# Kernel optimization log

Measured on AMD Instinct MI355X. Metric: run time of the kernel, lower is better.

Reference implementation:

```python
import jax, jax.numpy as jnp
import numpy as np

NUM_HEADS = 14
NUM_KV_HEADS = 2
HEAD_DIM = 64
HIDDEN = 896
ROPE_THETA = 1000000.0
NEG_INF = -1e9


def _rope_tables(seq_len, dtype=jnp.float32):
    inv_freq = 1.0 / (ROPE_THETA ** (jnp.arange(0, HEAD_DIM, 2, dtype=jnp.float32) / HEAD_DIM))
    t = jnp.arange(seq_len, dtype=jnp.float32)
    freqs = t[:, None] * inv_freq[None, :]          # [S, hd/2]
    emb = jnp.concatenate((freqs, freqs), axis=-1)  # [S, hd]
    return jnp.cos(emb).astype(dtype), jnp.sin(emb).astype(dtype)


def _rotate_half(x):
    x1, x2 = x[..., : x.shape[-1] // 2], x[..., x.shape[-1] // 2 :]
    return jnp.concatenate((-x2, x1), axis=-1)


def setup_inputs() -> dict:
    key = jax.random.key(0)
    ks = jax.random.split(key, 6)
    B, S = 2, 2048
    hidden_states = jax.random.normal(ks[0], (B, S, HIDDEN), dtype=jnp.float32)
    # additive causal mask [1, 1, S, S]
    causal = jnp.tril(jnp.ones((S, S), dtype=bool))
    attention_mask = jnp.where(causal, 0.0, NEG_INF).astype(jnp.float32)[None, None]
    sd = 1.0 / np.sqrt(HIDDEN)
    Wq = jax.random.normal(ks[1], (HIDDEN, NUM_HEADS * HEAD_DIM), dtype=jnp.float32) * sd
    bq = jnp.zeros((NUM_HEADS * HEAD_DIM,), dtype=jnp.float32)
    Wk = jax.random.normal(ks[2], (HIDDEN, NUM_KV_HEADS * HEAD_DIM), dtype=jnp.float32) * sd
    bk = jnp.zeros((NUM_KV_HEADS * HEAD_DIM,), dtype=jnp.float32)
    Wv = jax.random.normal(ks[3], (HIDDEN, NUM_KV_HEADS * HEAD_DIM), dtype=jnp.float32) * sd
    bv = jnp.zeros((NUM_KV_HEADS * HEAD_DIM,), dtype=jnp.float32)
    Wo = jax.random.normal(ks[4], (NUM_HEADS * HEAD_DIM, HIDDEN), dtype=jnp.float32) * sd
    return {
        'hidden_states': hidden_states, 'attention_mask': attention_mask,
        'Wq': Wq, 'bq': bq, 'Wk': Wk, 'bk': bk, 'Wv': Wv, 'bv': bv, 'Wo': Wo,
    }


def reference(hidden_states, attention_mask, Wq, bq, Wk, bk, Wv, bv, Wo):
    B, S, _ = hidden_states.shape
    n_groups = NUM_HEADS // NUM_KV_HEADS
    q = (hidden_states @ Wq + bq).reshape(B, S, NUM_HEADS, HEAD_DIM)
    k = (hidden_states @ Wk + bk).reshape(B, S, NUM_KV_HEADS, HEAD_DIM)
    v = (hidden_states @ Wv + bv).reshape(B, S, NUM_KV_HEADS, HEAD_DIM)

    cos, sin = _rope_tables(S, hidden_states.dtype)
    cos = cos[None, :, None, :]
    sin = sin[None, :, None, :]
    q = q * cos + _rotate_half(q) * sin
    k = k * cos + _rotate_half(k) * sin

    # GQA: repeat kv heads to match query heads
    k = jnp.repeat(k, n_groups, axis=2)  # [B, S, nH, hd]
    v = jnp.repeat(v, n_groups, axis=2)

    q = q.transpose(0, 2, 1, 3)  # [B, nH, S, hd]
    k = k.transpose(0, 2, 1, 3)
    v = v.transpose(0, 2, 1, 3)

    scores = jnp.einsum('bhqd,bhkd->bhqk', q, k) / jnp.sqrt(jnp.float32(HEAD_DIM)).astype(q.dtype)
    scores = scores + attention_mask
    attn = jax.nn.softmax(scores, axis=-1)
    out = jnp.einsum('bhqk,bhkd->bhqd', attn, v)        # [B, nH, S, hd]
    out = out.transpose(0, 2, 1, 3).reshape(B, S, -1)   # [B, S, nH*hd]
    return out @ Wo
```

## Files before the change

kernel.cpp:

```cpp
#include <hip/hip_runtime.h>
#include <hip/hip_bf16.h>
#include <math.h>

#define NH 14
#define NKV 2
#define HD 64
#define HID 896
#define SEQ 2048
#define BATCH 2
#define KT 28

typedef __attribute__((ext_vector_type(8))) short short8;
typedef __attribute__((ext_vector_type(4))) float f32x4;
typedef unsigned short ushort_t;

__device__ __forceinline__ unsigned short f2b(float f) {
    unsigned int u = __float_as_uint(f);
    unsigned int r = (u + 0x7fffu + ((u >> 16) & 1u)) >> 16;
    return (unsigned short)r;
}

__global__ __launch_bounds__(256) void xcast_kernel(
    const float* __restrict__ X, ushort_t* __restrict__ Xb)
{
    size_t i = ((size_t)blockIdx.x * 256 + threadIdx.x) * 8;
    float4 a = *(const float4*)(X + i);
    float4 b = *(const float4*)(X + i + 4);
    short8 o;
    o[0] = f2b(a.x); o[1] = f2b(a.y); o[2] = f2b(a.z); o[3] = f2b(a.w);
    o[4] = f2b(b.x); o[5] = f2b(b.y); o[6] = f2b(b.z); o[7] = f2b(b.w);
    *(short8*)(Xb + i) = o;
}

__global__ __launch_bounds__(256) void wtrans_kernel(
    const float* __restrict__ Wq, const float* __restrict__ Wk,
    const float* __restrict__ Wv, const float* __restrict__ Wo,
    ushort_t* __restrict__ WqkvT, ushort_t* __restrict__ WoT)
{
    __shared__ float tile[32][33];
    const int tx = threadIdx.x, ty = threadIdx.y;
    const int z = blockIdx.z;
    const float* src; ushort_t* dst; int N, rowoff;
    if      (z == 0) { src = Wq; dst = WqkvT; N = HID; rowoff = 0;    }
    else if (z == 1) { src = Wk; dst = WqkvT; N = 128; rowoff = 896;  }
    else if (z == 2) { src = Wv; dst = WqkvT; N = 128; rowoff = 1024; }
    else             { src = Wo; dst = WoT;   N = HID; rowoff = 0;    }
    const int k0 = blockIdx.x * 32;
    const int n0 = blockIdx.y * 32;
    if (n0 >= N) return;
    #pragma unroll
    for (int i = 0; i < 4; ++i)
        tile[ty * 4 + i][tx] = src[(size_t)(k0 + ty * 4 + i) * N + n0 + tx];
    __syncthreads();
    #pragma unroll
    for (int i = 0; i < 4; ++i)
        dst[(size_t)(rowoff + n0 + ty * 4 + i) * HID + k0 + tx]
            = f2b(tile[tx][ty * 4 + i]);
}

#define LDA 40
__global__ __launch_bounds__(256) void qkv_kernel(
    const ushort_t* __restrict__ Xb, const ushort_t* __restrict__ WqkvT,
    const float* __restrict__ bq, const float* __restrict__ bk,
    const float* __restrict__ bv,
    ushort_t* __restrict__ qbuf, ushort_t* __restrict__ kbuf,
    ushort_t* __restrict__ vbuf)
{
    __shared__ ushort_t Asb[2][128 * LDA];
    __shared__ ushort_t Bsb[2][64 * LDA];
    const int tid  = threadIdx.x;
    const int w    = tid >> 6;
    const int lane = tid & 63;
    const int quad = lane >> 4;
    const int l16  = lane & 15;
    const int m0 = blockIdx.x * 128;
    const int nt = blockIdx.y;
    const int nb = nt * 64;

    const int ar0 = tid >> 2;
    const int ac8 = tid & 3;
    const ushort_t* Ag0 = Xb + (size_t)(m0 + ar0) * HID + ac8 * 8;
    const ushort_t* Ag1 = Xb + (size_t)(m0 + ar0 + 64) * HID + ac8 * 8;
    const ushort_t* Bg  = WqkvT + (size_t)(nb + ar0) * HID + ac8 * 8;

    f32x4 acc[2][4];
    #pragma unroll
    for (int mf = 0; mf < 2; ++mf)
        #pragma unroll
        for (int nf = 0; nf < 4; ++nf) acc[mf][nf] = (f32x4){0.f, 0.f, 0.f, 0.f};

    short8 aReg0, aReg1, bReg;
    aReg0 = *(const short8*)(Ag0);
    aReg1 = *(const short8*)(Ag1);
    bReg  = *(const short8*)(Bg);
    *(short8*)&Asb[0][ar0 * LDA + ac8 * 8]        = aReg0;
    *(short8*)&Asb[0][(ar0 + 64) * LDA + ac8 * 8] = aReg1;
    *(short8*)&Bsb[0][ar0 * LDA + ac8 * 8]        = bReg;
    aReg0 = *(const short8*)(Ag0 + 32);
    aReg1 = *(const short8*)(Ag1 + 32);
    bReg  = *(const short8*)(Bg  + 32);

    for (int ks = 0; ks < KT; ++ks) {
        __syncthreads();
        const int cur = ks & 1;
        if (ks + 1 < KT) {
            *(short8*)&Asb[cur ^ 1][ar0 * LDA + ac8 * 8]        = aReg0;
            *(short8*)&Asb[cur ^ 1][(ar0 + 64) * LDA + ac8 * 8] = aReg1;
            *(short8*)&Bsb[cur ^ 1][ar0 * LDA + ac8 * 8]        = bReg;
        }
        if (ks + 2 < KT) {
            aReg0 = *(const short8*)(Ag0 + (ks + 2) * 32);
            aReg1 = *(const short8*)(Ag1 + (ks + 2) * 32);
            bReg  = *(const short8*)(Bg  + (ks + 2) * 32);
        }
        const ushort_t* Ab = &Asb[cur][(w * 32 + l16) * LDA + quad * 8];
        short8 a0 = *(const short8*)Ab;
        short8 a1 = *(const short8*)(Ab + 16 * LDA);
        #pragma unroll
        for (int nf = 0; nf < 4; ++nf) {
            short8 bf = *(const short8*)&Bsb[cur][(nf * 16 + l16) * LDA + quad * 8];
            acc[0][nf] = __builtin_amdgcn_mfma_f32_16x16x32_bf16(a0, bf, acc[0][nf], 0, 0, 0);
            acc[1][nf] = __builtin_amdgcn_mfma_f32_16x16x32_bf16(a1, bf, acc[1][nf], 0, 0, 0);
        }
    }

    float bcol[4];
    #pragma unroll
    for (int f = 0; f < 4; ++f) {
        int d = f * 16 + l16;
        bcol[f] = (nt < 14) ? bq[nt * 64 + d]
                : (nt < 16) ? bk[(nt - 14) * 64 + d]
                            : bv[(nt - 16) * 64 + d];
    }
    const float lnth = 13.815510558f;
    float if0 = expf(-((float)l16)        / 32.0f * lnth);
    float if1 = expf(-((float)(l16 + 16)) / 32.0f * lnth);

    #pragma unroll
    for (int mf = 0; mf < 2; ++mf)
        #pragma unroll
        for (int r = 0; r < 4; ++r) {
            int grow = m0 + w * 32 + mf * 16 + quad * 4 + r;
            int b = grow >> 11;
            int s = grow & 2047;
            float v0 = acc[mf][0][r] + bcol[0];
            float v1 = acc[mf][1][r] + bcol[1];
            float v2 = acc[mf][2][r] + bcol[2];
            float v3 = acc[mf][3][r] + bcol[3];
            if (nt < 16) {
                float s0, c0, s1, c1;
                sincosf((float)s * if0, &s0, &c0);
                sincosf((float)s * if1, &s1, &c1);
                float n0 = v0 * c0 - v2 * s0;
                float n2 = v2 * c0 + v0 * s0;
                float n1 = v1 * c1 - v3 * s1;
                float n3 = v3 * c1 + v1 * s1;
                v0 = n0; v1 = n1; v2 = n2; v3 = n3;
            }
            if (nt < 14) {
                ushort_t* dst = qbuf + ((size_t)(b * NH + nt) * SEQ + s) * HD;
                dst[l16]      = f2b(v0);
                dst[l16 + 16] = f2b(v1);
                dst[l16 + 32] = f2b(v2);
                dst[l16 + 48] = f2b(v3);
            } else if (nt < 16) {
                ushort_t* dst = kbuf + ((size_t)(b * NKV + nt - 14) * SEQ + s) * HD;
                dst[l16]      = f2b(v0);
                dst[l16 + 16] = f2b(v1);
                dst[l16 + 32] = f2b(v2);
                dst[l16 + 48] = f2b(v3);
            } else {
                ushort_t* dst = vbuf + (size_t)(b * NKV + nt - 16) * HD * SEQ + s;
                dst[(size_t)(l16)      * SEQ] = f2b(v0);
                dst[(size_t)(l16 + 16) * SEQ] = f2b(v1);
                dst[(size_t)(l16 + 32) * SEQ] = f2b(v2);
                dst[(size_t)(l16 + 48) * SEQ] = f2b(v3);
            }
        }
}

#define LDP 76
__global__ __launch_bounds__(256) void attn_kernel(
    const ushort_t* __restrict__ qbuf, const ushort_t* __restrict__ kbuf,
    const ushort_t* __restrict__ vbuf, ushort_t* __restrict__ abuf)
{
    __shared__ ushort_t Ks[64 * LDP];
    __shared__ ushort_t Vt[64 * LDP];
    __shared__ ushort_t Ps[4][16 * LDP];

    const int tid  = threadIdx.x;
    const int w    = tid >> 6;
    const int lane = tid & 63;
    const int quad = lane >> 4;
    const int l16  = lane & 15;
    const int bi = blockIdx.x;
    const int h  = blockIdx.y;
    const int b  = blockIdx.z;
    const int kvh = h / (NH / NKV);

    const ushort_t* kb_h = kbuf + (size_t)(b * NKV + kvh) * SEQ * HD;
    const ushort_t* vt_h = vbuf + (size_t)(b * NKV + kvh) * HD * SEQ;

    for (int pass = 0; pass < 2; ++pass) {
        const int qt = pass ? (31 - bi) : bi;

        const ushort_t* qrow =
            qbuf + ((size_t)((b * NH + h) * SEQ) + qt * 64 + w * 16 + l16) * HD;
        short8 qf0 = *(const short8*)(qrow + quad * 8);
        short8 qf1 = *(const short8*)(qrow + 32 + quad * 8);

        f32x4 O[4];
        float m_i[4], l_i[4];
        #pragma unroll
        for (int n = 0; n < 4; ++n) O[n] = (f32x4){0.f, 0.f, 0.f, 0.f};
        #pragma unroll
        for (int r = 0; r < 4; ++r) { m_i[r] = -1e30f; l_i[r] = 0.0f; }

        for (int kt = 0; kt <= qt; ++kt) {
            __syncthreads();
            for (int i = tid; i < 512; i += 256) {
                int row = i >> 3, c8 = i & 7;
                *(short8*)&Ks[row * LDP + c8 * 8] =
                    *(const short8*)(kb_h + ((size_t)(kt * 64 + row)) * HD + c8 * 8);
                *(short8*)&Vt[row * LDP + c8 * 8] =
                    *(const short8*)(vt_h + (size_t)row * SEQ + kt * 64 + c8 * 8);
            }
            __syncthreads();

            f32x4 S[4];
            #pragma unroll
            for (int f = 0; f < 4; ++f) {
                S[f] = (f32x4){0.f, 0.f, 0.f, 0.f};
                short8 kf0 = *(const short8*)&Ks[(f * 16 + l16) * LDP + quad * 8];
                short8 kf1 = *(const short8*)&Ks[(f * 16 + l16) * LDP + 32 + quad * 8];
                S[f] = __builtin_amdgcn_mfma_f32_16x16x32_bf16(qf0, kf0, S[f], 0, 0, 0);
                S[f] = __builtin_amdgcn_mfma_f32_16x16x32_bf16(qf1, kf1, S[f], 0, 0, 0);
            }

            const bool diag = (kt == qt);
            float sc[4][4];
            #pragma unroll
            for (int f = 0; f < 4; ++f)
                #pragma unroll
                for (int r = 0; r < 4; ++r) {
                    float v = S[f][r] * 0.125f;
                    if (diag && (f * 16 + l16) > (w * 16 + quad * 4 + r)) v = -1e30f;
                    sc[f][r] = v;
                }

            float pm[4];
            #pragma unroll
            for (int r = 0; r < 4; ++r)
                pm[r] = fmaxf(fmaxf(sc[0][r], sc[1][r]), fmaxf(sc[2][r], sc[3][r]));
            #pragma unroll
            for (int off = 1; off < 16; off <<= 1)
                #pragma unroll
                for (int r = 0; r < 4; ++r)
                    pm[r] = fmaxf(pm[r], __shfl_xor(pm[r], off));

            float alpha[4], psum[4];
            #pragma unroll
            for (int r = 0; r < 4; ++r) {
                float mnew = fmaxf(m_i[r], pm[r]);
                alpha[r] = __expf(m_i[r] - mnew);
                m_i[r] = mnew;
                psum[r] = 0.0f;
            }
            #pragma unroll
            for (int f = 0; f < 4; ++f)
                #pragma unroll
                for (int r = 0; r < 4; ++r) {
                    float p = __expf(sc[f][r] - m_i[r]);
                    sc[f][r] = p;
                    psum[r] += p;
                }
            #pragma unroll
            for (int off = 1; off < 16; off <<= 1)
                #pragma unroll
                for (int r = 0; r < 4; ++r)
                    psum[r] += __shfl_xor(psum[r], off);
            #pragma unroll
            for (int r = 0; r < 4; ++r)
                l_i[r] = l_i[r] * alpha[r] + psum[r];
            #pragma unroll
            for (int n = 0; n < 4; ++n)
                #pragma unroll
                for (int r = 0; r < 4; ++r)
                    O[n][r] *= alpha[r];

            #pragma unroll
            for (int f = 0; f < 4; ++f)
                #pragma unroll
                for (int r = 0; r < 4; ++r)
                    Ps[w][(quad * 4 + r) * LDP + f * 16 + l16] = f2b(sc[f][r]);
            short8 pa0 = *(const short8*)&Ps[w][l16 * LDP + quad * 8];
            short8 pa1 = *(const short8*)&Ps[w][l16 * LDP + 32 + quad * 8];

            #pragma unroll
            for (int n = 0; n < 4; ++n) {
                short8 vf0 = *(const short8*)&Vt[(n * 16 + l16) * LDP + quad * 8];
                short8 vf1 = *(const short8*)&Vt[(n * 16 + l16) * LDP + 32 + quad * 8];
                O[n] = __builtin_amdgcn_mfma_f32_16x16x32_bf16(pa0, vf0, O[n], 0, 0, 0);
                O[n] = __builtin_amdgcn_mfma_f32_16x16x32_bf16(pa1, vf1, O[n], 0, 0, 0);
            }
        }

        float inv[4];
        #pragma unroll
        for (int r = 0; r < 4; ++r) inv[r] = 1.0f / l_i[r];
        #pragma unroll
        for (int n = 0; n < 4; ++n)
            #pragma unroll
            for (int r = 0; r < 4; ++r) {
                int rowg = qt * 64 + w * 16 + quad * 4 + r;
                abuf[(size_t)(b * SEQ + rowg) * HID + h * HD + n * 16 + l16]
                    = f2b(O[n][r] * inv[r]);
            }
    }
}

__global__ __launch_bounds__(256) void oproj_kernel(
    const ushort_t* __restrict__ A, const ushort_t* __restrict__ WoT,
    float* __restrict__ out)
{
    __shared__ ushort_t Asb[2][128 * LDA];
    __shared__ ushort_t Bsb[2][64 * LDA];
    const int tid  = threadIdx.x;
    const int w    = tid >> 6;
    const int lane = tid & 63;
    const int quad = lane >> 4;
    const int l16  = lane & 15;
    const int m0 = blockIdx.x * 128;
    const int n0 = blockIdx.y * 64;

    const int ar0 = tid >> 2;
    const int ac8 = tid & 3;
    const ushort_t* Ag0 = A + (size_t)(m0 + ar0) * HID + ac8 * 8;
    const ushort_t* Ag1 = A + (size_t)(m0 + ar0 + 64) * HID + ac8 * 8;
    const ushort_t* Bg  = WoT + (size_t)(n0 + ar0) * HID + ac8 * 8;

    f32x4 acc[2][4];
    #pragma unroll
    for (int mf = 0; mf < 2; ++mf)
        #pragma unroll
        for (int nf = 0; nf < 4; ++nf) acc[mf][nf] = (f32x4){0.f, 0.f, 0.f, 0.f};

    short8 aReg0, aReg1, bReg;
    aReg0 = *(const short8*)(Ag0);
    aReg1 = *(const short8*)(Ag1);
    bReg  = *(const short8*)(Bg);
    *(short8*)&Asb[0][ar0 * LDA + ac8 * 8]        = aReg0;
    *(short8*)&Asb[0][(ar0 + 64) * LDA + ac8 * 8] = aReg1;
    *(short8*)&Bsb[0][ar0 * LDA + ac8 * 8]        = bReg;
    aReg0 = *(const short8*)(Ag0 + 32);
    aReg1 = *(const short8*)(Ag1 + 32);
    bReg  = *(const short8*)(Bg  + 32);

    for (int ks = 0; ks < KT; ++ks) {
        __syncthreads();
        const int cur = ks & 1;
        if (ks + 1 < KT) {
            *(short8*)&Asb[cur ^ 1][ar0 * LDA + ac8 * 8]        = aReg0;
            *(short8*)&Asb[cur ^ 1][(ar0 + 64) * LDA + ac8 * 8] = aReg1;
            *(short8*)&Bsb[cur ^ 1][ar0 * LDA + ac8 * 8]        = bReg;
        }
        if (ks + 2 < KT) {
            aReg0 = *(const short8*)(Ag0 + (ks + 2) * 32);
            aReg1 = *(const short8*)(Ag1 + (ks + 2) * 32);
            bReg  = *(const short8*)(Bg  + (ks + 2) * 32);
        }
        const ushort_t* Ab = &Asb[cur][(w * 32 + l16) * LDA + quad * 8];
        short8 a0 = *(const short8*)Ab;
        short8 a1 = *(const short8*)(Ab + 16 * LDA);
        #pragma unroll
        for (int nf = 0; nf < 4; ++nf) {
            short8 bf = *(const short8*)&Bsb[cur][(nf * 16 + l16) * LDA + quad * 8];
            acc[0][nf] = __builtin_amdgcn_mfma_f32_16x16x32_bf16(a0, bf, acc[0][nf], 0, 0, 0);
            acc[1][nf] = __builtin_amdgcn_mfma_f32_16x16x32_bf16(a1, bf, acc[1][nf], 0, 0, 0);
        }
    }

    #pragma unroll
    for (int mf = 0; mf < 2; ++mf)
        #pragma unroll
        for (int r = 0; r < 4; ++r) {
            size_t rbase = (size_t)(m0 + w * 32 + mf * 16 + quad * 4 + r) * HID + n0;
            #pragma unroll
            for (int f = 0; f < 4; ++f)
                out[rbase + f * 16 + l16] = acc[mf][f][r];
        }
}

extern "C" void kernel_launch(void* const* d_in, const int* in_sizes, int n_in,
                              void* d_out, int out_size, void* d_ws, size_t ws_size,
                              hipStream_t stream) {
    const float* X  = (const float*)d_in[0];
    const float* Wq = (const float*)d_in[2];
    const float* bq = (const float*)d_in[3];
    const float* Wk = (const float*)d_in[4];
    const float* bk = (const float*)d_in[5];
    const float* Wv = (const float*)d_in[6];
    const float* bv = (const float*)d_in[7];
    const float* Wo = (const float*)d_in[8];
    float* out = (float*)d_out;

    ushort_t* ws    = (ushort_t*)d_ws;
    ushort_t* Xb    = ws;
    ushort_t* WqkvT = Xb    + 3670016;
    ushort_t* WoT   = WqkvT + 1032192;
    ushort_t* qbuf  = WoT   + 802816;
    ushort_t* kbuf  = qbuf  + 3670016;
    ushort_t* vbuf  = kbuf  + 524288;
    ushort_t* abufb = vbuf  + 524288;

    xcast_kernel<<<dim3(1792), 256, 0, stream>>>(X, Xb);
    wtrans_kernel<<<dim3(28, 28, 4), dim3(32, 8), 0, stream>>>(
        Wq, Wk, Wv, Wo, WqkvT, WoT);
    qkv_kernel<<<dim3(32, 18), 256, 0, stream>>>(
        Xb, WqkvT, bq, bk, bv, qbuf, kbuf, vbuf);
    attn_kernel<<<dim3(16, NH, BATCH), 256, 0, stream>>>(
        qbuf, kbuf, vbuf, abufb);
    oproj_kernel<<<dim3(32, 14), 256, 0, stream>>>(
        abufb, WoT, out);
}
```

Baseline: 209.5 us.

## Load K/V fragments directly from global, drop LDS staging and pass pairing

The attention kernel stops staging K and V tiles through shared memory with two block barriers per step. Each wave now loads its MFMA fragments straight from global memory, relying on cache reuse across waves. The grid doubles to one query tile per block instead of pairing tiles for load balance. The 1/sqrt(d) scale is folded into Q in the projection kernel, and softmax uses exp2 with a log2e prescale. Risks are redundant global/L2 traffic across the four waves and causal-imbalanced blocks.

```diff
diff --git a/kernel.cpp b/kernel.cpp
--- a/kernel.cpp
+++ b/kernel.cpp
@@ -18,6 +18,10 @@
     unsigned int u = __float_as_uint(f);
     unsigned int r = (u + 0x7fffu + ((u >> 16) & 1u)) >> 16;
     return (unsigned short)r;
+}
+
+__device__ __forceinline__ float exp2fast(float x) {
+    return __builtin_amdgcn_exp2f(x);
 }
 
 __global__ __launch_bounds__(256) void xcast_kernel(
@@ -158,6 +162,7 @@
                 v0 = n0; v1 = n1; v2 = n2; v3 = n3;
             }
             if (nt < 14) {
+                v0 *= 0.125f; v1 *= 0.125f; v2 *= 0.125f; v3 *= 0.125f;
                 ushort_t* dst = qbuf + ((size_t)(b * NH + nt) * SEQ + s) * HD;
                 dst[l16]      = f2b(v0);
                 dst[l16 + 16] = f2b(v1);
@@ -184,8 +189,6 @@
     const ushort_t* __restrict__ qbuf, const ushort_t* __restrict__ kbuf,
     const ushort_t* __restrict__ vbuf, ushort_t* __restrict__ abuf)
 {
-    __shared__ ushort_t Ks[64 * LDP];
-    __shared__ ushort_t Vt[64 * LDP];
     __shared__ ushort_t Ps[4][16 * LDP];
 
     const int tid  = threadIdx.x;
@@ -193,7 +196,7 @@
     const int lane = tid & 63;
     const int quad = lane >> 4;
     const int l16  = lane & 15;
-    const int bi = blockIdx.x;
+    const int qt = blockIdx.x;
     const int h  = blockIdx.y;
     const int b  = blockIdx.z;
     const int kvh = h / (NH / NKV);
@@ -201,122 +204,121 @@
     const ushort_t* kb_h = kbuf + (size_t)(b * NKV + kvh) * SEQ * HD;
     const ushort_t* vt_h = vbuf + (size_t)(b * NKV + kvh) * HD * SEQ;
 
-    for (int pass = 0; pass < 2; ++pass) {
-        const int qt = pass ? (31 - bi) : bi;
-
-        const ushort_t* qrow =
-            qbuf + ((size_t)((b * NH + h) * SEQ) + qt * 64 + w * 16 + l16) * HD;
-        short8 qf0 = *(const short8*)(qrow + quad * 8);
-        short8 qf1 = *(const short8*)(qrow + 32 + quad * 8);
-
-        f32x4 O[4];
-        float m_i[4], l_i[4];
-        #pragma unroll
-        for (int n = 0; n < 4; ++n) O[n] = (f32x4){0.f, 0.f, 0.f, 0.f};
-        #pragma unroll
-        for (int r = 0; r < 4; ++r) { m_i[r] = -1e30f; l_i[r] = 0.0f; }
-
-        for (int kt = 0; kt <= qt; ++kt) {
-            __syncthreads();
-            for (int i = tid; i < 512; i += 256) {
-                int row = i >> 3, c8 = i & 7;
-                *(short8*)&Ks[row * LDP + c8 * 8] =
-                    *(const short8*)(kb_h + ((size_t)(kt * 64 + row)) * HD + c8 * 8);
-                *(short8*)&Vt[row * LDP + c8 * 8] =
-                    *(const short8*)(vt_h + (size_t)row * SEQ + kt * 64 + c8 * 8);
-            }
-            __syncthreads();
-
-            f32x4 S[4];
-            #pragma unroll
-            for (int f = 0; f < 4; ++f) {
-                S[f] = (f32x4){0.f, 0.f, 0.f, 0.f};
-                short8 kf0 = *(const short8*)&Ks[(f * 16 + l16) * LDP + quad * 8];
-                short8 kf1 = *(const short8*)&Ks[(f * 16 + l16) * LDP + 32 + quad * 8];
-                S[f] = __builtin_amdgcn_mfma_f32_16x16x32_bf16(qf0, kf0, S[f], 0, 0, 0);
-                S[f] = __builtin_amdgcn_mfma_f32_16x16x32_bf16(qf1, kf1, S[f], 0, 0, 0);
-            }
-
-            const bool diag = (kt == qt);
-            float sc[4][4];
-            #pragma unroll
-            for (int f = 0; f < 4; ++f)
-                #pragma unroll
-                for (int r = 0; r < 4; ++r) {
-                    float v = S[f][r] * 0.125f;
-                    if (diag && (f * 16 + l16) > (w * 16 + quad * 4 + r)) v = -1e30f;
-                    sc[f][r] = v;
-                }
-
-            float pm[4];
+    const ushort_t* qrow =
+        qbuf + ((size_t)((b * NH + h) * SEQ) + qt * 64 + w * 16 + l16) * HD;
+    short8 qf0 = *(const short8*)(qrow + quad * 8);
+    short8 qf1 = *(const short8*)(qrow + 32 + quad * 8);
+
+    f32x4 O[4];
+    float m_i[4], l_i[4];
+    #pragma unroll
+    for (int n = 0; n < 4; ++n) O[n] = (f32x4){0.f, 0.f, 0.f, 0.f};
+    #pragma unroll
+    for (int r = 0; r < 4; ++r) { m_i[r] = -1e30f; l_i[r] = 0.0f; }
+
+    for (int kt = 0; kt <= qt; ++kt) {
+        f32x4 S[4];
+        #pragma unroll
+        for (int f = 0; f < 4; ++f) {
+            const ushort_t* kp =
+                kb_h + ((size_t)(kt * 64 + f * 16 + l16)) * HD + quad * 8;
+            short8 kf0 = *(const short8*)kp;
+            short8 kf1 = *(const short8*)(kp + 32);
+            S[f] = (f32x4){0.f, 0.f, 0.f, 0.f};
+            S[f] = __builtin_amdgcn_mfma_f32_16x16x32_bf16(qf0, kf0, S[f], 0, 0, 0);
+            S[f] = __builtin_amdgcn_mfma_f32_16x16x32_bf16(qf1, kf1, S[f], 0, 0, 0);
+        }
+
+        short8 vfr[4][2];
+        #pragma unroll
+        for (int n = 0; n < 4; ++n) {
+            const ushort_t* vp =
+                vt_h + (size_t)(n * 16 + l16) * SEQ + (size_t)kt * 64 + quad * 8;
+            vfr[n][0] = *(const short8*)vp;
+            vfr[n][1] = *(const short8*)(vp + 32);
+        }
+
+        float sc[4][4];
+        #pragma unroll
+        for (int f = 0; f < 4; ++f)
             #pragma unroll
             for (int r = 0; r < 4; ++r)
-                pm[r] = fmaxf(fmaxf(sc[0][r], sc[1][r]), fmaxf(sc[2][r], sc[3][r]));
-            #pragma unroll
-            for (int off = 1; off < 16; off <<= 1)
-                #pragma unroll
-                for (int r = 0; r < 4; ++r)
-                    pm[r] = fmaxf(pm[r], __shfl_xor(pm[r], off));
-
-            float alpha[4], psum[4];
-            #pragma unroll
-            for (int r = 0; r < 4; ++r) {
-                float mnew = fmaxf(m_i[r], pm[r]);
-                alpha[r] = __expf(m_i[r] - mnew);
-                m_i[r] = mnew;
-                psum[r] = 0.0f;
-            }
-            #pragma unroll
-            for (int f = 0; f < 4; ++f)
-                #pragma unroll
-                for (int r = 0; r < 4; ++r) {
-                    float p = __expf(sc[f][r] - m_i[r]);
-                    sc[f][r] = p;
-                    psum[r] += p;
-                }
-            #pragma unroll
-            for (int off = 1; off < 16; off <<= 1)
-                #pragma unroll
-                for (int r = 0; r < 4; ++r)
-                    psum[r] += __shfl_xor(psum[r], off);
-            #pragma unroll
-            for (int r = 0; r < 4; ++r)
-                l_i[r] = l_i[r] * alpha[r] + psum[r];
-            #pragma unroll
-            for (int n = 0; n < 4; ++n)
-                #pragma unroll
-                for (int r = 0; r < 4; ++r)
-                    O[n][r] *= alpha[r];
-
+                sc[f][r] = S[f][r] * 1.44269504f;
+        if (kt == qt) {
             #pragma unroll
             for (int f = 0; f < 4; ++f)
                 #pragma unroll
                 for (int r = 0; r < 4; ++r)
-                    Ps[w][(quad * 4 + r) * LDP + f * 16 + l16] = f2b(sc[f][r]);
-            short8 pa0 = *(const short8*)&Ps[w][l16 * LDP + quad * 8];
-            short8 pa1 = *(const short8*)&Ps[w][l16 * LDP + 32 + quad * 8];
-
-            #pragma unroll
-            for (int n = 0; n < 4; ++n) {
-                short8 vf0 = *(const short8*)&Vt[(n * 16 + l16) * LDP + quad * 8];
-                short8 vf1 = *(const short8*)&Vt[(n * 16 + l16) * LDP + 32 + quad * 8];
-                O[n] = __builtin_amdgcn_mfma_f32_16x16x32_bf16(pa0, vf0, O[n], 0, 0, 0);
-                O[n] = __builtin_amdgcn_mfma_f32_16x16x32_bf16(pa1, vf1, O[n], 0, 0, 0);
+                    if ((f * 16 + l16) > (w * 16 + quad * 4 + r))
+                        sc[f][r] = -1e30f;
+        }
+
+        float pm[4];
+        #pragma unroll
+        for (int r = 0; r < 4; ++r)
+            pm[r] = fmaxf(fmaxf(sc[0][r], sc[1][r]), fmaxf(sc[2][r], sc[3][r]));
+        #pragma unroll
+        for (int off = 1; off < 16; off <<= 1)
+            #pragma unroll
+            for (int r = 0; r < 4; ++r)
+                pm[r] = fmaxf(pm[r], __shfl_xor(pm[r], off));
+
+        float alpha[4], psum[4];
+        #pragma unroll
+        for (int r = 0; r < 4; ++r) {
+            float mnew = fmaxf(m_i[r], pm[r]);
+            alpha[r] = exp2fast(m_i[r] - mnew);
+            m_i[r] = mnew;
+            psum[r] = 0.0f;
+        }
+        #pragma unroll
+        for (int f = 0; f < 4; ++f)
+            #pragma unroll
+            for (int r = 0; r < 4; ++r) {
+                float p = exp2fast(sc[f][r] - m_i[r]);
+                sc[f][r] = p;
+                psum[r] += p;
             }
-        }
-
-        float inv[4];
-        #pragma unroll
-        for (int r = 0; r < 4; ++r) inv[r] = 1.0f / l_i[r];
+        #pragma unroll
+        for (int off = 1; off < 16; off <<= 1)
+            #pragma unroll
+            for (int r = 0; r < 4; ++r)
+                psum[r] += __shfl_xor(psum[r], off);
+        #pragma unroll
+        for (int r = 0; r < 4; ++r)
+            l_i[r] = l_i[r] * alpha[r] + psum[r];
         #pragma unroll
         for (int n = 0; n < 4; ++n)
             #pragma unroll
-            for (int r = 0; r < 4; ++r) {
-                int rowg = qt * 64 + w * 16 + quad * 4 + r;
-                abuf[(size_t)(b * SEQ + rowg) * HID + h * HD + n * 16 + l16]
-                    = f2b(O[n][r] * inv[r]);
-            }
+            for (int r = 0; r < 4; ++r)
+                O[n][r] *= alpha[r];
+
+        #pragma unroll
+        for (int f = 0; f < 4; ++f)
+            #pragma unroll
+            for (int r = 0; r < 4; ++r)
+                Ps[w][(quad * 4 + r) * LDP + f * 16 + l16] = f2b(sc[f][r]);
+        short8 pa0 = *(const short8*)&Ps[w][l16 * LDP + quad * 8];
+        short8 pa1 = *(const short8*)&Ps[w][l16 * LDP + 32 + quad * 8];
+
+        #pragma unroll
+        for (int n = 0; n < 4; ++n) {
+            O[n] = __builtin_amdgcn_mfma_f32_16x16x32_bf16(pa0, vfr[n][0], O[n], 0, 0, 0);
+            O[n] = __builtin_amdgcn_mfma_f32_16x16x32_bf16(pa1, vfr[n][1], O[n], 0, 0, 0);
+        }
     }
+
+    float inv[4];
+    #pragma unroll
+    for (int r = 0; r < 4; ++r) inv[r] = 1.0f / l_i[r];
+    #pragma unroll
+    for (int n = 0; n < 4; ++n)
+        #pragma unroll
+        for (int r = 0; r < 4; ++r) {
+            int rowg = qt * 64 + w * 16 + quad * 4 + r;
+            abuf[(size_t)(b * SEQ + rowg) * HID + h * HD + n * 16 + l16]
+                = f2b(O[n][r] * inv[r]);
+        }
 }
 
 __global__ __launch_bounds__(256) void oproj_kernel(
@@ -418,7 +420,7 @@
         Wq, Wk, Wv, Wo, WqkvT, WoT);
     qkv_kernel<<<dim3(32, 18), 256, 0, stream>>>(
         Xb, WqkvT, bq, bk, bv, qbuf, kbuf, vbuf);
-    attn_kernel<<<dim3(16, NH, BATCH), 256, 0, stream>>>(
+    attn_kernel<<<dim3(32, NH, BATCH), 256, 0, stream>>>(
         qbuf, kbuf, vbuf, abufb);
     oproj_kernel<<<dim3(32, 14), 256, 0, stream>>>(
         abufb, WoT, out);
```

New measurement: 372.8 us. 77.9% more time.

## Prefetch next K/V tile into registers and use exp2 softmax with prescaled Q

Applied to the files above, without the earlier changes.

Global loads of the next K and V tile are issued into registers right after the shared-memory barrier, so they overlap with the current tile's MFMA and softmax work instead of stalling before each tile. The 1/sqrt(d) scale is folded into Q during the projection epilogue, and softmax uses the native exp2 with a log2(e) multiply in place of __expf. The causal mask is applied only on the diagonal tile, as a separate branch. The cost is more live registers and an extra bf16 rounding of the scaled Q values.

```diff
diff --git a/kernel.cpp b/kernel.cpp
--- a/kernel.cpp
+++ b/kernel.cpp
@@ -18,6 +18,10 @@
     unsigned int u = __float_as_uint(f);
     unsigned int r = (u + 0x7fffu + ((u >> 16) & 1u)) >> 16;
     return (unsigned short)r;
+}
+
+__device__ __forceinline__ float exp2fast(float x) {
+    return __builtin_amdgcn_exp2f(x);
 }
 
 __global__ __launch_bounds__(256) void xcast_kernel(
@@ -158,6 +162,7 @@
                 v0 = n0; v1 = n1; v2 = n2; v3 = n3;
             }
             if (nt < 14) {
+                v0 *= 0.125f; v1 *= 0.125f; v2 *= 0.125f; v3 *= 0.125f;
                 ushort_t* dst = qbuf + ((size_t)(b * NH + nt) * SEQ + s) * HD;
                 dst[l16]      = f2b(v0);
                 dst[l16 + 16] = f2b(v1);
@@ -201,6 +206,13 @@
     const ushort_t* kb_h = kbuf + (size_t)(b * NKV + kvh) * SEQ * HD;
     const ushort_t* vt_h = vbuf + (size_t)(b * NKV + kvh) * HD * SEQ;
 
+    const int srow = tid >> 3;
+    const int sc8  = tid & 7;
+    const ushort_t* Kg0 = kb_h + (size_t)srow * HD + sc8 * 8;
+    const ushort_t* Kg1 = kb_h + (size_t)(srow + 32) * HD + sc8 * 8;
+    const ushort_t* Vg0 = vt_h + (size_t)srow * SEQ + sc8 * 8;
+    const ushort_t* Vg1 = vt_h + (size_t)(srow + 32) * SEQ + sc8 * 8;
+
     for (int pass = 0; pass < 2; ++pass) {
         const int qt = pass ? (31 - bi) : bi;
 
@@ -216,37 +228,49 @@
         #pragma unroll
         for (int r = 0; r < 4; ++r) { m_i[r] = -1e30f; l_i[r] = 0.0f; }
 
+        short8 kr0 = *(const short8*)(Kg0);
+        short8 kr1 = *(const short8*)(Kg1);
+        short8 vr0 = *(const short8*)(Vg0);
+        short8 vr1 = *(const short8*)(Vg1);
+
         for (int kt = 0; kt <= qt; ++kt) {
             __syncthreads();
-            for (int i = tid; i < 512; i += 256) {
-                int row = i >> 3, c8 = i & 7;
-                *(short8*)&Ks[row * LDP + c8 * 8] =
-                    *(const short8*)(kb_h + ((size_t)(kt * 64 + row)) * HD + c8 * 8);
-                *(short8*)&Vt[row * LDP + c8 * 8] =
-                    *(const short8*)(vt_h + (size_t)row * SEQ + kt * 64 + c8 * 8);
-            }
+            *(short8*)&Ks[srow * LDP + sc8 * 8]        = kr0;
+            *(short8*)&Ks[(srow + 32) * LDP + sc8 * 8] = kr1;
+            *(short8*)&Vt[srow * LDP + sc8 * 8]        = vr0;
+            *(short8*)&Vt[(srow + 32) * LDP + sc8 * 8] = vr1;
             __syncthreads();
+            if (kt < qt) {
+                kr0 = *(const short8*)(Kg0 + (size_t)(kt + 1) * 64 * HD);
+                kr1 = *(const short8*)(Kg1 + (size_t)(kt + 1) * 64 * HD);
+                vr0 = *(const short8*)(Vg0 + (kt + 1) * 64);
+                vr1 = *(const short8*)(Vg1 + (kt + 1) * 64);
+            }
 
             f32x4 S[4];
             #pragma unroll
             for (int f = 0; f < 4; ++f) {
-                S[f] = (f32x4){0.f, 0.f, 0.f, 0.f};
                 short8 kf0 = *(const short8*)&Ks[(f * 16 + l16) * LDP + quad * 8];
                 short8 kf1 = *(const short8*)&Ks[(f * 16 + l16) * LDP + 32 + quad * 8];
+                S[f] = (f32x4){0.f, 0.f, 0.f, 0.f};
                 S[f] = __builtin_amdgcn_mfma_f32_16x16x32_bf16(qf0, kf0, S[f], 0, 0, 0);
                 S[f] = __builtin_amdgcn_mfma_f32_16x16x32_bf16(qf1, kf1, S[f], 0, 0, 0);
             }
 
-            const bool diag = (kt == qt);
             float sc[4][4];
             #pragma unroll
             for (int f = 0; f < 4; ++f)
                 #pragma unroll
-                for (int r = 0; r < 4; ++r) {
-                    float v = S[f][r] * 0.125f;
-                    if (diag && (f * 16 + l16) > (w * 16 + quad * 4 + r)) v = -1e30f;
-                    sc[f][r] = v;
-                }
+                for (int r = 0; r < 4; ++r)
+                    sc[f][r] = S[f][r] * 1.44269504f;
+            if (kt == qt) {
+                #pragma unroll
+                for (int f = 0; f < 4; ++f)
+                    #pragma unroll
+                    for (int r = 0; r < 4; ++r)
+                        if ((f * 16 + l16) > (w * 16 + quad * 4 + r))
+                            sc[f][r] = -1e30f;
+            }
 
             float pm[4];
             #pragma unroll
@@ -262,7 +286,7 @@
             #pragma unroll
             for (int r = 0; r < 4; ++r) {
                 float mnew = fmaxf(m_i[r], pm[r]);
-                alpha[r] = __expf(m_i[r] - mnew);
+                alpha[r] = exp2fast(m_i[r] - mnew);
                 m_i[r] = mnew;
                 psum[r] = 0.0f;
             }
@@ -270,7 +294,7 @@
             for (int f = 0; f < 4; ++f)
                 #pragma unroll
                 for (int r = 0; r < 4; ++r) {
-                    float p = __expf(sc[f][r] - m_i[r]);
+                    float p = exp2fast(sc[f][r] - m_i[r]);
                     sc[f][r] = p;
                     psum[r] += p;
                 }
```

New measurement: 198.9 us. 1.05x faster.
